# Optimization experiments

Hardware: AMD Instinct MI355X
Metric: run time of the kernel (lower is better)

## Reference

```python
import jax, jax.numpy as jnp
import numpy as np

N_NODES = 100000
N_EDGES = 600000
DIM = 128
N_BEHAVIORS = 4


def setup_inputs() -> dict:
    key = jax.random.key(0)
    ks = jax.random.split(key, 10)
    user = jax.random.randint(ks[0], (N_NODES,), 0, N_NODES, dtype=jnp.int32)
    item = jax.random.randint(ks[1], (N_NODES,), 0, N_NODES, dtype=jnp.int32)
    behavior = jax.random.randint(ks[2], (N_NODES,), 0, N_BEHAVIORS, dtype=jnp.int32)
    adj_rows = jax.random.randint(ks[3], (N_EDGES,), 0, N_NODES, dtype=jnp.int32)
    adj_cols = jax.random.randint(ks[4], (N_EDGES,), 0, N_NODES, dtype=jnp.int32)
    adj_vals = jax.random.uniform(ks[5], (N_EDGES,), dtype=jnp.float32)
    user_table = jax.random.normal(ks[6], (N_NODES, DIM), dtype=jnp.float32)
    item_table = jax.random.normal(ks[7], (N_NODES, DIM), dtype=jnp.float32)
    behavior_table = jax.random.normal(ks[8], (N_BEHAVIORS, DIM), dtype=jnp.float32)
    kw, kb = jax.random.split(ks[9])
    bound = 1.0 / np.sqrt(DIM)
    W = jax.random.uniform(kw, (DIM, DIM), minval=-bound, maxval=bound, dtype=jnp.float32)
    b = jax.random.uniform(kb, (DIM,), minval=-bound, maxval=bound, dtype=jnp.float32)
    return {"user": user, "item": item, "behavior": behavior,
            "adj_rows": adj_rows, "adj_cols": adj_cols, "adj_vals": adj_vals,
            "user_table": user_table, "item_table": item_table,
            "behavior_table": behavior_table, "W": W, "b": b}


def reference(user, item, behavior, adj_rows, adj_cols, adj_vals,
              user_table, item_table, behavior_table, W, b):
    # embedding sum: [N, D]
    x = user_table[user] + item_table[item] + behavior_table[behavior]
    # sparse adjacency matmul: out[r] = sum_e adj_vals[e] * x[cols[e]] for rows[e]==r
    msg = adj_vals[:, None] * x[adj_cols]                       # [E, D]
    agg = jax.ops.segment_sum(msg, adj_rows, num_segments=N_NODES)  # [N, D]
    # dense linear
    return agg @ W.T + b
```

## Files before the change

kernel.cpp:

```cpp
#include <hip/hip_runtime.h>

#define N_NODES 100000
#define N_EDGES 600000
#define DIM 128

#define N4 (N_NODES / 4)
#define SCAN_BLOCKS ((N_NODES + 1023) / 1024)

#define HIST_B  2344
#define WCONV_B 16
#define BUCKET_B 2344
#define FUSED_B  1563

typedef __attribute__((ext_vector_type(8))) short bf16x8;
typedef __attribute__((ext_vector_type(4))) float f32x4;

__device__ __forceinline__ void fma4(float4& acc, float s, const float4 w) {
    acc.x = fmaf(s, w.x, acc.x);
    acc.y = fmaf(s, w.y, acc.y);
    acc.z = fmaf(s, w.z, acc.z);
    acc.w = fmaf(s, w.w, acc.w);
}

__device__ __forceinline__ unsigned short f2bf(float f) {
    union { float f; unsigned int u; } v; v.f = f;
    unsigned int r = v.u + 0x7fffu + ((v.u >> 16) & 1u);
    return (unsigned short)(r >> 16);
}

__device__ __forceinline__ float bf2f(unsigned short u) {
    union { unsigned int i; float f; } v;
    v.i = ((unsigned int)u) << 16;
    return v.f;
}

__global__ __launch_bounds__(256) void hw_kernel(
    const int* __restrict__ rows, int* __restrict__ cnt,
    const float* __restrict__ W, unsigned short* __restrict__ wfrag)
{
    int b = blockIdx.x;
    int t = threadIdx.x;
    if (b < HIST_B) {
        int e = b * 256 + t;
        if (e < N_EDGES) atomicAdd(&cnt[rows[e]], 1);
    } else {
        int c4 = (b - HIST_B) * 256 + t;
        if (c4 < 128 * 128 / 4) {
            float4 wv = ((const float4*)W)[c4];
            int i  = c4 >> 5;
            int k0 = (c4 & 31) * 4;
            int slot = (i >> 4) * 4 + (k0 >> 5);
            int lane = ((k0 & 31) >> 3) * 16 + (i & 15);
            ushort4 o;
            o.x = f2bf(wv.x); o.y = f2bf(wv.y); o.z = f2bf(wv.z); o.w = f2bf(wv.w);
            *(ushort4*)&wfrag[slot * 512 + lane * 8 + (k0 & 7)] = o;
        }
    }
}

__global__ __launch_bounds__(256) void scan1_kernel(
    const int* __restrict__ cnt, int* __restrict__ off, int* __restrict__ bsum)
{
    __shared__ int s[256];
    int t = threadIdx.x;
    int b = blockIdx.x;
    int i4 = b * 256 + t;
    int4 c = {0, 0, 0, 0};
    if (i4 < N4) c = ((const int4*)cnt)[i4];
    int tsum = c.x + c.y + c.z + c.w;
    s[t] = tsum;
    __syncthreads();
    for (int d = 1; d < 256; d <<= 1) {
        int v = (t >= d) ? s[t - d] : 0;
        __syncthreads();
        s[t] += v;
        __syncthreads();
    }
    int texcl = s[t] - tsum;
    if (t == 255) bsum[b] = s[255];
    if (i4 < N4) {
        int4 o;
        o.x = texcl;
        o.y = o.x + c.x;
        o.z = o.y + c.y;
        o.w = o.z + c.z;
        ((int4*)off)[i4] = o;
    }
}

__global__ __launch_bounds__(256) void scan3_kernel(
    const int* __restrict__ bsum, int* __restrict__ off, int* __restrict__ cur)
{
    __shared__ int s[256];
    int t = threadIdx.x;
    int b = blockIdx.x;
    s[t] = (t < b && t < SCAN_BLOCKS) ? bsum[t] : 0;
    __syncthreads();
    for (int d = 1; d < 256; d <<= 1) {
        int v = (t >= d) ? s[t - d] : 0;
        __syncthreads();
        s[t] += v;
        __syncthreads();
    }
    int base = s[255];
    int i4 = b * 256 + t;
    if (i4 < N4) {
        int4 o = ((const int4*)off)[i4];
        o.x += base; o.y += base; o.z += base; o.w += base;
        ((int4*)off)[i4] = o;
        ((int4*)cur)[i4] = o;
    }
    if (b == 0 && t == 0) off[N_NODES] = N_EDGES;
}

__global__ __launch_bounds__(256) void kb_kernel(
    const int* __restrict__ rows, const int* __restrict__ cols, const float* __restrict__ vals,
    int* __restrict__ cur, int2* __restrict__ epack,
    const int* __restrict__ user, const int* __restrict__ item, const int* __restrict__ behavior,
    const float* __restrict__ ut, const float* __restrict__ itb, const float* __restrict__ bt,
    const bf16x8* __restrict__ wf, unsigned short* __restrict__ y)
{
    int b = blockIdx.x;
    int t = threadIdx.x;
    if (b < BUCKET_B) {
        int e = b * 256 + t;
        if (e < N_EDGES) {
            int r = rows[e];
            int slot = atomicAdd(&cur[r], 1);
            int2 p;
            p.x = cols[e];
            p.y = __float_as_int(vals[e]);
            epack[slot] = p;
        }
    } else {
        int b2 = b - BUCKET_B;
        int l = t & 63;
        int w = t >> 6;
        int c = l & 15;
        int g = l >> 4;
        int row = b2 * 64 + w * 16 + c;
        int rowc = row < N_NODES ? row : N_NODES - 1;

        int u  = user[rowc];
        int iv = item[rowc];
        int bh = behavior[rowc];
        const float4* ut4 = (const float4*)ut;
        const float4* it4 = (const float4*)itb;
        const float4* bt4 = (const float4*)bt;

        bf16x8 bfrag[4];
        #pragma unroll
        for (int s = 0; s < 4; ++s) {
            int base = 8 * s + 2 * g;
            float4 a0 = ut4[(size_t)u  * 32 + base];
            float4 a1 = ut4[(size_t)u  * 32 + base + 1];
            float4 c0 = it4[(size_t)iv * 32 + base];
            float4 c1 = it4[(size_t)iv * 32 + base + 1];
            float4 d0 = bt4[(size_t)bh * 32 + base];
            float4 d1 = bt4[(size_t)bh * 32 + base + 1];
            bf16x8 tt;
            tt[0] = (short)f2bf(a0.x + c0.x + d0.x);
            tt[1] = (short)f2bf(a0.y + c0.y + d0.y);
            tt[2] = (short)f2bf(a0.z + c0.z + d0.z);
            tt[3] = (short)f2bf(a0.w + c0.w + d0.w);
            tt[4] = (short)f2bf(a1.x + c1.x + d1.x);
            tt[5] = (short)f2bf(a1.y + c1.y + d1.y);
            tt[6] = (short)f2bf(a1.z + c1.z + d1.z);
            tt[7] = (short)f2bf(a1.w + c1.w + d1.w);
            bfrag[s] = tt;
        }

        f32x4 acc[8];
        #pragma unroll
        for (int ti = 0; ti < 8; ++ti) acc[ti] = (f32x4){0.f, 0.f, 0.f, 0.f};

        #pragma unroll
        for (int ti = 0; ti < 8; ++ti) {
            #pragma unroll
            for (int s = 0; s < 4; ++s) {
                bf16x8 af = wf[(ti * 4 + s) * 64 + l];
                acc[ti] = __builtin_amdgcn_mfma_f32_16x16x32_bf16(af, bfrag[s], acc[ti], 0, 0, 0);
            }
        }

        if (row < N_NODES) {
            unsigned short* yr = y + (size_t)row * DIM;
            #pragma unroll
            for (int ti = 0; ti < 8; ++ti) {
                ushort4 o;
                o.x = f2bf(acc[ti][0]);
                o.y = f2bf(acc[ti][1]);
                o.z = f2bf(acc[ti][2]);
                o.w = f2bf(acc[ti][3]);
                *(ushort4*)(yr + 16 * ti + 4 * g) = o;
            }
        }
    }
}

__global__ __launch_bounds__(256) void agg_bias_kernel(
    const int* __restrict__ off, const int2* __restrict__ epack,
    const unsigned short* __restrict__ y, const float* __restrict__ bias,
    float* __restrict__ out)
{
    int gid = blockIdx.x * 256 + threadIdx.x;
    int r = gid >> 4;
    int m = gid & 15;
    if (r >= N_NODES) return;
    int s = off[r], e = off[r + 1];
    const bf16x8* y8 = (const bf16x8*)y;

    float a0[8], a1[8], a2[8], a3[8];
    #pragma unroll
    for (int j = 0; j < 8; ++j) { a0[j] = 0.f; a1[j] = 0.f; a2[j] = 0.f; a3[j] = 0.f; }

    int i = s;
    for (; i + 3 < e; i += 4) {
        int2 p0 = epack[i];
        int2 p1 = epack[i + 1];
        int2 p2 = epack[i + 2];
        int2 p3 = epack[i + 3];
        bf16x8 y0 = y8[(size_t)p0.x * 16 + m];
        bf16x8 y1 = y8[(size_t)p1.x * 16 + m];
        bf16x8 y2 = y8[(size_t)p2.x * 16 + m];
        bf16x8 y3 = y8[(size_t)p3.x * 16 + m];
        float v0 = __int_as_float(p0.y);
        float v1 = __int_as_float(p1.y);
        float v2 = __int_as_float(p2.y);
        float v3 = __int_as_float(p3.y);
        #pragma unroll
        for (int j = 0; j < 8; ++j) {
            a0[j] = fmaf(v0, bf2f((unsigned short)y0[j]), a0[j]);
            a1[j] = fmaf(v1, bf2f((unsigned short)y1[j]), a1[j]);
            a2[j] = fmaf(v2, bf2f((unsigned short)y2[j]), a2[j]);
            a3[j] = fmaf(v3, bf2f((unsigned short)y3[j]), a3[j]);
        }
    }
    for (; i < e; ++i) {
        int2 p0 = epack[i];
        float v0 = __int_as_float(p0.y);
        bf16x8 y0 = y8[(size_t)p0.x * 16 + m];
        #pragma unroll
        for (int j = 0; j < 8; ++j)
            a0[j] = fmaf(v0, bf2f((unsigned short)y0[j]), a0[j]);
    }

    const float4* b4 = (const float4*)bias;
    float4 bb0 = b4[2 * m], bb1 = b4[2 * m + 1];
    float4 o0, o1;
    o0.x = a0[0] + a1[0] + a2[0] + a3[0] + bb0.x;
    o0.y = a0[1] + a1[1] + a2[1] + a3[1] + bb0.y;
    o0.z = a0[2] + a1[2] + a2[2] + a3[2] + bb0.z;
    o0.w = a0[3] + a1[3] + a2[3] + a3[3] + bb0.w;
    o1.x = a0[4] + a1[4] + a2[4] + a3[4] + bb1.x;
    o1.y = a0[5] + a1[5] + a2[5] + a3[5] + bb1.y;
    o1.z = a0[6] + a1[6] + a2[6] + a3[6] + bb1.z;
    o1.w = a0[7] + a1[7] + a2[7] + a3[7] + bb1.w;
    float4* orow = (float4*)(out + (size_t)r * DIM);
    orow[2 * m]     = o0;
    orow[2 * m + 1] = o1;
}


__global__ __launch_bounds__(256) void hist_kernel(
    const int* __restrict__ rows, int* __restrict__ cnt)
{
    int e = blockIdx.x * 256 + threadIdx.x;
    if (e >= N_EDGES) return;
    atomicAdd(&cnt[rows[e]], 1);
}

__global__ __launch_bounds__(256) void bucket_kernel(
    const int* __restrict__ rows, const int* __restrict__ cols, const float* __restrict__ vals,
    int* __restrict__ cur, int2* __restrict__ epack)
{
    int e = blockIdx.x * 256 + threadIdx.x;
    if (e >= N_EDGES) return;
    int r = rows[e];
    int slot = atomicAdd(&cur[r], 1);
    int2 p;
    p.x = cols[e];
    p.y = __float_as_int(vals[e]);
    epack[slot] = p;
}

__global__ __launch_bounds__(256) void agg_fused_kernel(
    const int* __restrict__ off, const int2* __restrict__ epack,
    const int* __restrict__ user, const int* __restrict__ item, const int* __restrict__ behavior,
    const float* __restrict__ ut, const float* __restrict__ itb, const float* __restrict__ bt,
    float* __restrict__ out)
{
    int gid = blockIdx.x * 256 + threadIdx.x;
    int r = gid >> 5;
    int m = gid & 31;
    if (r >= N_NODES) return;
    int s = off[r], e = off[r + 1];
    const float4* ut4 = (const float4*)ut;
    const float4* it4 = (const float4*)itb;
    const float4* bt4 = (const float4*)bt;
    float4 acc = {0.f, 0.f, 0.f, 0.f};
    for (int i = s; i < e; ++i) {
        int2 p = epack[i];
        int c = p.x;
        float v = __int_as_float(p.y);
        float4 a = ut4[(size_t)user[c] * 32 + m];
        float4 cc = it4[(size_t)item[c] * 32 + m];
        float4 d = bt4[(size_t)behavior[c] * 32 + m];
        a.x += cc.x + d.x; a.y += cc.y + d.y; a.z += cc.z + d.z; a.w += cc.w + d.w;
        fma4(acc, v, a);
    }
    ((float4*)out)[(size_t)r * 32 + m] = acc;
}

__global__ __launch_bounds__(256) void scatter_fused_kernel(
    const int* __restrict__ rows, const int* __restrict__ cols, const float* __restrict__ vals,
    const int* __restrict__ user, const int* __restrict__ item, const int* __restrict__ behavior,
    const float* __restrict__ ut, const float* __restrict__ itb, const float* __restrict__ bt,
    float* __restrict__ agg)
{
    int wave = (blockIdx.x * 256 + threadIdx.x) >> 6;
    int lane = threadIdx.x & 63;
    int e = wave * 2 + (lane >> 5);
    if (e >= N_EDGES) return;
    int r = rows[e];
    int c = cols[e];
    float v = vals[e];
    int m = lane & 31;
    const float4* ut4 = (const float4*)ut;
    const float4* it4 = (const float4*)itb;
    const float4* bt4 = (const float4*)bt;
    float4 a = ut4[(size_t)user[c] * 32 + m];
    float4 cc = it4[(size_t)item[c] * 32 + m];
    float4 d = bt4[(size_t)behavior[c] * 32 + m];
    a.x += cc.x + d.x; a.y += cc.y + d.y; a.z += cc.z + d.z; a.w += cc.w + d.w;
    float* o = agg + (size_t)r * DIM + m * 4;
    atomicAdd(o + 0, v * a.x);
    atomicAdd(o + 1, v * a.y);
    atomicAdd(o + 2, v * a.z);
    atomicAdd(o + 3, v * a.w);
}

__global__ __launch_bounds__(256) void gemm_mfma_kernel(
    const float* __restrict__ W, const float* __restrict__ bias, float* io)
{
    __shared__ unsigned short wlds[128 * 128];

    int tid = threadIdx.x;
    for (int c4 = tid; c4 < 128 * 128 / 4; c4 += 256) {
        float4 wv = ((const float4*)W)[c4];
        int i  = c4 >> 5;
        int k0 = (c4 & 31) * 4;
        int slot = (i >> 4) * 4 + (k0 >> 5);
        int lane = ((k0 & 31) >> 3) * 16 + (i & 15);
        ushort4 o;
        o.x = f2bf(wv.x); o.y = f2bf(wv.y); o.z = f2bf(wv.z); o.w = f2bf(wv.w);
        *(ushort4*)&wlds[slot * 512 + lane * 8 + (k0 & 7)] = o;
    }
    __syncthreads();

    int l = tid & 63;
    int w = tid >> 6;
    int c = l & 15;
    int g = l >> 4;
    int row = blockIdx.x * 64 + w * 16 + c;
    int rowc = row < N_NODES ? row : N_NODES - 1;

    const float4* a4 = (const float4*)io;
    bf16x8 bfrag[4];
    #pragma unroll
    for (int s = 0; s < 4; ++s) {
        float4 p0 = a4[(size_t)rowc * 32 + 8 * s + 2 * g];
        float4 p1 = a4[(size_t)rowc * 32 + 8 * s + 2 * g + 1];
        bf16x8 t;
        t[0] = (short)f2bf(p0.x); t[1] = (short)f2bf(p0.y);
        t[2] = (short)f2bf(p0.z); t[3] = (short)f2bf(p0.w);
        t[4] = (short)f2bf(p1.x); t[5] = (short)f2bf(p1.y);
        t[6] = (short)f2bf(p1.z); t[7] = (short)f2bf(p1.w);
        bfrag[s] = t;
    }

    f32x4 acc[8];
    #pragma unroll
    for (int ti = 0; ti < 8; ++ti) acc[ti] = (f32x4){0.f, 0.f, 0.f, 0.f};

    const bf16x8* wf = (const bf16x8*)wlds;
    #pragma unroll
    for (int ti = 0; ti < 8; ++ti) {
        #pragma unroll
        for (int s = 0; s < 4; ++s) {
            bf16x8 af = wf[(ti * 4 + s) * 64 + l];
            acc[ti] = __builtin_amdgcn_mfma_f32_16x16x32_bf16(af, bfrag[s], acc[ti], 0, 0, 0);
        }
    }

    if (row < N_NODES) {
        float4* orow = (float4*)(io + (size_t)row * DIM);
        const float4* b4 = (const float4*)bias;
        #pragma unroll
        for (int ti = 0; ti < 8; ++ti) {
            float4 bb = b4[ti * 4 + g];
            float4 o;
            o.x = acc[ti][0] + bb.x;
            o.y = acc[ti][1] + bb.y;
            o.z = acc[ti][2] + bb.z;
            o.w = acc[ti][3] + bb.w;
            orow[ti * 4 + g] = o;
        }
    }
}

extern "C" void kernel_launch(void* const* d_in, const int* in_sizes, int n_in,
                              void* d_out, int out_size, void* d_ws, size_t ws_size,
                              hipStream_t stream) {
    const int*   user           = (const int*)d_in[0];
    const int*   item           = (const int*)d_in[1];
    const int*   behavior       = (const int*)d_in[2];
    const int*   adj_rows       = (const int*)d_in[3];
    const int*   adj_cols       = (const int*)d_in[4];
    const float* adj_vals       = (const float*)d_in[5];
    const float* user_table     = (const float*)d_in[6];
    const float* item_table     = (const float*)d_in[7];
    const float* behavior_table = (const float*)d_in[8];
    const float* W              = (const float*)d_in[9];
    const float* b              = (const float*)d_in[10];
    float* out = (float*)d_out;

    const size_t Y_BYTES     = (size_t)N_NODES * DIM * sizeof(unsigned short);
    const size_t CNT_BYTES   = (size_t)N_NODES * sizeof(int);
    const size_t OFF_BYTES   = ((size_t)(N_NODES + 1) * sizeof(int) + 15) & ~(size_t)15;
    const size_t EPACK_BYTES = (size_t)N_EDGES * sizeof(int2);
    const size_t WFRAG_BYTES = 128 * 128 * sizeof(unsigned short);

    const int edge_blocks = (N_EDGES + 255) / 256;
    const int agg_blocks  = (N_NODES * 16 + 255) / 256;
    const int gemm_blocks = (N_NODES + 63) / 64;

    char* ws = (char*)d_ws;
    const size_t need_full = Y_BYTES + CNT_BYTES + OFF_BYTES + EPACK_BYTES + WFRAG_BYTES;
    const size_t need_csr  = CNT_BYTES + OFF_BYTES + EPACK_BYTES;

    if (ws_size >= need_full) {
        size_t o = 0;
        unsigned short* y = (unsigned short*)(ws + o); o += Y_BYTES;
        int*  cnt   = (int*)(ws + o); o += CNT_BYTES;
        int*  off   = (int*)(ws + o); o += OFF_BYTES;
        int2* epack = (int2*)(ws + o); o += EPACK_BYTES;
        unsigned short* wfrag = (unsigned short*)(ws + o);
        int*  bsum  = (int*)epack;

        hipMemsetAsync(cnt, 0, CNT_BYTES, stream);
        hw_kernel<<<HIST_B + WCONV_B, 256, 0, stream>>>(adj_rows, cnt, W, wfrag);
        scan1_kernel<<<SCAN_BLOCKS, 256, 0, stream>>>(cnt, off, bsum);
        scan3_kernel<<<SCAN_BLOCKS, 256, 0, stream>>>(bsum, off, cnt);
        kb_kernel<<<BUCKET_B + FUSED_B, 256, 0, stream>>>(
            adj_rows, adj_cols, adj_vals, cnt, epack,
            user, item, behavior, user_table, item_table, behavior_table,
            (const bf16x8*)wfrag, y);
        agg_bias_kernel<<<agg_blocks, 256, 0, stream>>>(off, epack, y, b, out);
    } else if (ws_size >= need_csr) {
        int*  cnt   = (int*)ws;
        int*  off   = (int*)(ws + CNT_BYTES);
        int2* epack = (int2*)(ws + CNT_BYTES + OFF_BYTES);
        int*  bsum  = (int*)epack;

        hipMemsetAsync(cnt, 0, CNT_BYTES, stream);
        hist_kernel<<<edge_blocks, 256, 0, stream>>>(adj_rows, cnt);
        scan1_kernel<<<SCAN_BLOCKS, 256, 0, stream>>>(cnt, off, bsum);
        scan3_kernel<<<SCAN_BLOCKS, 256, 0, stream>>>(bsum, off, cnt);
        bucket_kernel<<<edge_blocks, 256, 0, stream>>>(
            adj_rows, adj_cols, adj_vals, cnt, epack);
        agg_fused_kernel<<<(N_NODES * 32 + 255) / 256, 256, 0, stream>>>(
            off, epack, user, item, behavior,
            user_table, item_table, behavior_table, out);
        gemm_mfma_kernel<<<gemm_blocks, 256, 0, stream>>>(W, b, out);
    } else {
        hipMemsetAsync(d_out, 0, (size_t)N_NODES * DIM * sizeof(float), stream);
        const int scatter_blocks = (N_EDGES / 2 * 64 + 255) / 256;
        scatter_fused_kernel<<<scatter_blocks, 256, 0, stream>>>(
            adj_rows, adj_cols, adj_vals, user, item, behavior,
            user_table, item_table, behavior_table, out);
        gemm_mfma_kernel<<<gemm_blocks, 256, 0, stream>>>(W, b, out);
    }
}
```

Measured before the change: 155.0 us.

## Pre-transform embedding tables by W, then gather-sum projected rows; partition bucketing

Instead of gathering and summing the three embedding rows and then multiplying by W per node, the linear map is applied once to the whole user, item and behavior tables. The projected tables are stored as bf16 in the output buffer, and the per-node work becomes a cheap gather-and-add of projected rows. The bucketing pass is also split into 8 row partitions per edge chunk, aiming for better locality of the cursor atomics and epack writes. In exchange it does two full-table GEMMs of 100k rows each instead of one, converts W to bf16 inside every tile, and rounds to bf16 twice, which changes numerics.

```diff
diff --git a/kernel.cpp b/kernel.cpp
--- a/kernel.cpp
+++ b/kernel.cpp
@@ -8,9 +8,12 @@
 #define SCAN_BLOCKS ((N_NODES + 1023) / 1024)
 
 #define HIST_B  2344
-#define WCONV_B 16
-#define BUCKET_B 2344
-#define FUSED_B  1563
+#define TCONV_B 1563
+#define NPART    8
+#define CHUNKS   ((N_EDGES + 1023) / 1024)
+#define BUCKET_B (CHUNKS * NPART)
+#define COMBINE_B 6250
+#define PART_SZ  (N_NODES / NPART)
 
 typedef __attribute__((ext_vector_type(8))) short bf16x8;
 typedef __attribute__((ext_vector_type(4))) float f32x4;
@@ -34,27 +37,84 @@
     return v.f;
 }
 
-__global__ __launch_bounds__(256) void hw_kernel(
+__device__ __forceinline__ void tconv_tile(
+    const float* __restrict__ T, unsigned short* __restrict__ TW, int NT,
+    const float* __restrict__ W, int base, int t)
+{
+    int l = t & 63;
+    int w = t >> 6;
+    int c = l & 15;
+    int g = l >> 4;
+    int row = base + w * 16 + c;
+    int rowc = row < NT ? row : NT - 1;
+    const float4* T4 = (const float4*)T;
+    const float4* W4 = (const float4*)W;
+
+    bf16x8 bfrag[4];
+    #pragma unroll
+    for (int s = 0; s < 4; ++s) {
+        float4 p0 = T4[(size_t)rowc * 32 + 8 * s + 2 * g];
+        float4 p1 = T4[(size_t)rowc * 32 + 8 * s + 2 * g + 1];
+        bf16x8 tt;
+        tt[0] = (short)f2bf(p0.x); tt[1] = (short)f2bf(p0.y);
+        tt[2] = (short)f2bf(p0.z); tt[3] = (short)f2bf(p0.w);
+        tt[4] = (short)f2bf(p1.x); tt[5] = (short)f2bf(p1.y);
+        tt[6] = (short)f2bf(p1.z); tt[7] = (short)f2bf(p1.w);
+        bfrag[s] = tt;
+    }
+
+    f32x4 acc[8];
+    #pragma unroll
+    for (int ti = 0; ti < 8; ++ti) acc[ti] = (f32x4){0.f, 0.f, 0.f, 0.f};
+
+    #pragma unroll
+    for (int ti = 0; ti < 8; ++ti) {
+        int wrow = 16 * ti + c;
+        #pragma unroll
+        for (int s = 0; s < 4; ++s) {
+            float4 w0 = W4[wrow * 32 + 8 * s + 2 * g];
+            float4 w1 = W4[wrow * 32 + 8 * s + 2 * g + 1];
+            bf16x8 af;
+            af[0] = (short)f2bf(w0.x); af[1] = (short)f2bf(w0.y);
+            af[2] = (short)f2bf(w0.z); af[3] = (short)f2bf(w0.w);
+            af[4] = (short)f2bf(w1.x); af[5] = (short)f2bf(w1.y);
+            af[6] = (short)f2bf(w1.z); af[7] = (short)f2bf(w1.w);
+            acc[ti] = __builtin_amdgcn_mfma_f32_16x16x32_bf16(af, bfrag[s], acc[ti], 0, 0, 0);
+        }
+    }
+
+    if (row < NT) {
+        unsigned short* yr = TW + (size_t)row * DIM;
+        #pragma unroll
+        for (int ti = 0; ti < 8; ++ti) {
+            ushort4 o;
+            o.x = f2bf(acc[ti][0]);
+            o.y = f2bf(acc[ti][1]);
+            o.z = f2bf(acc[ti][2]);
+            o.w = f2bf(acc[ti][3]);
+            *(ushort4*)(yr + 16 * ti + 4 * g) = o;
+        }
+    }
+}
+
+__global__ __launch_bounds__(256) void ka_kernel(
     const int* __restrict__ rows, int* __restrict__ cnt,
-    const float* __restrict__ W, unsigned short* __restrict__ wfrag)
+    const float* __restrict__ ut, const float* __restrict__ itb, const float* __restrict__ bt,
+    const float* __restrict__ W,
+    unsigned short* __restrict__ utw, unsigned short* __restrict__ itw,
+    unsigned short* __restrict__ btw)
 {
     int b = blockIdx.x;
     int t = threadIdx.x;
     if (b < HIST_B) {
         int e = b * 256 + t;
         if (e < N_EDGES) atomicAdd(&cnt[rows[e]], 1);
+    } else if (b < HIST_B + TCONV_B) {
+        tconv_tile(ut, utw, N_NODES, W, (b - HIST_B) * 64, t);
+    } else if (b < HIST_B + 2 * TCONV_B) {
+        tconv_tile(itb, itw, N_NODES, W, (b - HIST_B - TCONV_B) * 64, t);
     } else {
-        int c4 = (b - HIST_B) * 256 + t;
-        if (c4 < 128 * 128 / 4) {
-            float4 wv = ((const float4*)W)[c4];
-            int i  = c4 >> 5;
-            int k0 = (c4 & 31) * 4;
-            int slot = (i >> 4) * 4 + (k0 >> 5);
-            int lane = ((k0 & 31) >> 3) * 16 + (i & 15);
-            ushort4 o;
-            o.x = f2bf(wv.x); o.y = f2bf(wv.y); o.z = f2bf(wv.z); o.w = f2bf(wv.w);
-            *(ushort4*)&wfrag[slot * 512 + lane * 8 + (k0 & 7)] = o;
-        }
+        tconv_tile(bt, btw, 4, W, 0, t);
     }
 }
 
@@ -117,83 +177,51 @@
     const int* __restrict__ rows, const int* __restrict__ cols, const float* __restrict__ vals,
     int* __restrict__ cur, int2* __restrict__ epack,
     const int* __restrict__ user, const int* __restrict__ item, const int* __restrict__ behavior,
-    const float* __restrict__ ut, const float* __restrict__ itb, const float* __restrict__ bt,
-    const bf16x8* __restrict__ wf, unsigned short* __restrict__ y)
+    const unsigned short* __restrict__ utw, const unsigned short* __restrict__ itw,
+    const unsigned short* __restrict__ btw, unsigned short* __restrict__ y)
 {
     int b = blockIdx.x;
     int t = threadIdx.x;
     if (b < BUCKET_B) {
-        int e = b * 256 + t;
-        if (e < N_EDGES) {
-            int r = rows[e];
-            int slot = atomicAdd(&cur[r], 1);
-            int2 p;
-            p.x = cols[e];
-            p.y = __float_as_int(vals[e]);
-            epack[slot] = p;
+        int p = b & (NPART - 1);
+        int chunk = b >> 3;
+        int base = chunk * 1024;
+        #pragma unroll
+        for (int j = 0; j < 4; ++j) {
+            int e = base + t + j * 256;
+            if (e < N_EDGES) {
+                int r = rows[e];
+                if (r / PART_SZ == p) {
+                    int slot = atomicAdd(&cur[r], 1);
+                    int2 pk;
+                    pk.x = cols[e];
+                    pk.y = __float_as_int(vals[e]);
+                    epack[slot] = pk;
+                }
+            }
         }
     } else {
-        int b2 = b - BUCKET_B;
-        int l = t & 63;
-        int w = t >> 6;
-        int c = l & 15;
-        int g = l >> 4;
-        int row = b2 * 64 + w * 16 + c;
-        int rowc = row < N_NODES ? row : N_NODES - 1;
-
-        int u  = user[rowc];
-        int iv = item[rowc];
-        int bh = behavior[rowc];
-        const float4* ut4 = (const float4*)ut;
-        const float4* it4 = (const float4*)itb;
-        const float4* bt4 = (const float4*)bt;
-
-        bf16x8 bfrag[4];
-        #pragma unroll
-        for (int s = 0; s < 4; ++s) {
-            int base = 8 * s + 2 * g;
-            float4 a0 = ut4[(size_t)u  * 32 + base];
-            float4 a1 = ut4[(size_t)u  * 32 + base + 1];
-            float4 c0 = it4[(size_t)iv * 32 + base];
-            float4 c1 = it4[(size_t)iv * 32 + base + 1];
-            float4 d0 = bt4[(size_t)bh * 32 + base];
-            float4 d1 = bt4[(size_t)bh * 32 + base + 1];
-            bf16x8 tt;
-            tt[0] = (short)f2bf(a0.x + c0.x + d0.x);
-            tt[1] = (short)f2bf(a0.y + c0.y + d0.y);
-            tt[2] = (short)f2bf(a0.z + c0.z + d0.z);
-            tt[3] = (short)f2bf(a0.w + c0.w + d0.w);
-            tt[4] = (short)f2bf(a1.x + c1.x + d1.x);
-            tt[5] = (short)f2bf(a1.y + c1.y + d1.y);
-            tt[6] = (short)f2bf(a1.z + c1.z + d1.z);
-            tt[7] = (short)f2bf(a1.w + c1.w + d1.w);
-            bfrag[s] = tt;
-        }
-
-        f32x4 acc[8];
-        #pragma unroll
-        for (int ti = 0; ti < 8; ++ti) acc[ti] = (f32x4){0.f, 0.f, 0.f, 0.f};
-
-        #pragma unroll
-        for (int ti = 0; ti < 8; ++ti) {
+        int gid = (b - BUCKET_B) * 256 + t;
+        int r = gid >> 4;
+        int m = gid & 15;
+        if (r < N_NODES) {
+            int u  = user[r];
+            int iv = item[r];
+            int bh = behavior[r];
+            const bf16x8* U8 = (const bf16x8*)utw;
+            const bf16x8* I8 = (const bf16x8*)itw;
+            const bf16x8* B8 = (const bf16x8*)btw;
+            bf16x8 au = U8[(size_t)u  * 16 + m];
+            bf16x8 ai = I8[(size_t)iv * 16 + m];
+            bf16x8 ab = B8[bh * 16 + m];
+            bf16x8 o;
             #pragma unroll
-            for (int s = 0; s < 4; ++s) {
-                bf16x8 af = wf[(ti * 4 + s) * 64 + l];
-                acc[ti] = __builtin_amdgcn_mfma_f32_16x16x32_bf16(af, bfrag[s], acc[ti], 0, 0, 0);
+            for (int j = 0; j < 8; ++j) {
+                float f = bf2f((unsigned short)au[j]) + bf2f((unsigned short)ai[j])
+                        + bf2f((unsigned short)ab[j]);
+                o[j] = (short)f2bf(f);
             }
-        }
-
-        if (row < N_NODES) {
-            unsigned short* yr = y + (size_t)row * DIM;
-            #pragma unroll
-            for (int ti = 0; ti < 8; ++ti) {
-                ushort4 o;
-                o.x = f2bf(acc[ti][0]);
-                o.y = f2bf(acc[ti][1]);
-                o.z = f2bf(acc[ti][2]);
-                o.w = f2bf(acc[ti][3]);
-                *(ushort4*)(yr + 16 * ti + 4 * g) = o;
-            }
+            ((bf16x8*)y)[(size_t)r * 16 + m] = o;
         }
     }
 }
@@ -425,37 +453,40 @@
     const float* b              = (const float*)d_in[10];
     float* out = (float*)d_out;
 
-    const size_t Y_BYTES     = (size_t)N_NODES * DIM * sizeof(unsigned short);
+    const size_t TW_BYTES    = (size_t)N_NODES * DIM * sizeof(unsigned short);
+    const size_t Y_BYTES     = TW_BYTES;
     const size_t CNT_BYTES   = (size_t)N_NODES * sizeof(int);
     const size_t OFF_BYTES   = ((size_t)(N_NODES + 1) * sizeof(int) + 15) & ~(size_t)15;
     const size_t EPACK_BYTES = (size_t)N_EDGES * sizeof(int2);
-    const size_t WFRAG_BYTES = 128 * 128 * sizeof(unsigned short);
+    const size_t BTW_BYTES   = 1024;
 
     const int edge_blocks = (N_EDGES + 255) / 256;
     const int agg_blocks  = (N_NODES * 16 + 255) / 256;
     const int gemm_blocks = (N_NODES + 63) / 64;
 
     char* ws = (char*)d_ws;
-    const size_t need_full = Y_BYTES + CNT_BYTES + OFF_BYTES + EPACK_BYTES + WFRAG_BYTES;
+    const size_t need_full = Y_BYTES + CNT_BYTES + OFF_BYTES + EPACK_BYTES + BTW_BYTES;
     const size_t need_csr  = CNT_BYTES + OFF_BYTES + EPACK_BYTES;
 
     if (ws_size >= need_full) {
+        unsigned short* utw = (unsigned short*)d_out;
+        unsigned short* itw = utw + (size_t)N_NODES * DIM;
         size_t o = 0;
         unsigned short* y = (unsigned short*)(ws + o); o += Y_BYTES;
         int*  cnt   = (int*)(ws + o); o += CNT_BYTES;
         int*  off   = (int*)(ws + o); o += OFF_BYTES;
         int2* epack = (int2*)(ws + o); o += EPACK_BYTES;
-        unsigned short* wfrag = (unsigned short*)(ws + o);
+        unsigned short* btw = (unsigned short*)(ws + o);
         int*  bsum  = (int*)epack;
 
         hipMemsetAsync(cnt, 0, CNT_BYTES, stream);
-        hw_kernel<<<HIST_B + WCONV_B, 256, 0, stream>>>(adj_rows, cnt, W, wfrag);
+        ka_kernel<<<HIST_B + 2 * TCONV_B + 1, 256, 0, stream>>>(
+            adj_rows, cnt, user_table, item_table, behavior_table, W, utw, itw, btw);
         scan1_kernel<<<SCAN_BLOCKS, 256, 0, stream>>>(cnt, off, bsum);
         scan3_kernel<<<SCAN_BLOCKS, 256, 0, stream>>>(bsum, off, cnt);
-        kb_kernel<<<BUCKET_B + FUSED_B, 256, 0, stream>>>(
+        kb_kernel<<<BUCKET_B + COMBINE_B, 256, 0, stream>>>(
             adj_rows, adj_cols, adj_vals, cnt, epack,
-            user, item, behavior, user_table, item_table, behavior_table,
-            (const bf16x8*)wfrag, y);
+            user, item, behavior, utw, itw, btw, y);
         agg_bias_kernel<<<agg_blocks, 256, 0, stream>>>(off, epack, y, b, out);
     } else if (ws_size >= need_csr) {
         int*  cnt   = (int*)ws;
```

New measurement: 221.8 us. 1.43x slower.
